# Performance work log

Hardware: AMD Instinct MI355X
Metric: run time of the kernel (lower is better)

The kernel has to match this reference:

```python
import jax, jax.numpy as jnp
import numpy as np

VOCAB = 50257
EMB = 512
HID = 1024
H = HID // 2  # per-direction hidden
TAGS = 24
START = 22
STOP = 23
SEQ = 4096
NEG = -10000.0


def setup_inputs() -> dict:
    key = jax.random.key(0)
    ks = jax.random.split(key, 16)
    s = 1.0 / np.sqrt(H)
    u = lambda k, shp: jax.random.uniform(k, shp, jnp.float32, -s, s)
    sentence = jax.random.randint(ks[0], (SEQ,), 0, VOCAB)
    emb = jax.random.normal(ks[1], (VOCAB, EMB), jnp.float32)
    w_ih_f = u(ks[2], (4 * H, EMB)); w_hh_f = u(ks[3], (4 * H, H))
    b_ih_f = u(ks[4], (4 * H,));    b_hh_f = u(ks[5], (4 * H,))
    w_ih_b = u(ks[6], (4 * H, EMB)); w_hh_b = u(ks[7], (4 * H, H))
    b_ih_b = u(ks[8], (4 * H,));    b_hh_b = u(ks[9], (4 * H,))
    w_tag = u(ks[10], (TAGS, HID)); b_tag = u(ks[11], (TAGS,))
    transitions = jax.random.normal(ks[12], (TAGS, TAGS), jnp.float32)
    transitions = transitions.at[START, :].set(NEG).at[:, STOP].set(NEG)
    h0 = jax.random.normal(ks[13], (2, H), jnp.float32)  # [dir, H]
    c0 = jax.random.normal(ks[14], (2, H), jnp.float32)
    return dict(sentence=sentence, emb=emb,
                w_ih_f=w_ih_f, w_hh_f=w_hh_f, b_ih_f=b_ih_f, b_hh_f=b_hh_f,
                w_ih_b=w_ih_b, w_hh_b=w_hh_b, b_ih_b=b_ih_b, b_hh_b=b_hh_b,
                w_tag=w_tag, b_tag=b_tag, transitions=transitions, h0=h0, c0=c0)


def _lstm_dir(x, w_ih, w_hh, b_ih, b_hh, h, c, reverse):
    # x: [T, EMB]; precompute input projections once
    xg = x @ w_ih.T + (b_ih + b_hh)  # [T, 4H]
    def step(carry, xt):
        h, c = carry
        g = xt + h @ w_hh.T
        i, f, gg, o = jnp.split(g, 4)
        i = jax.nn.sigmoid(i); f = jax.nn.sigmoid(f)
        gg = jnp.tanh(gg);     o = jax.nn.sigmoid(o)
        c = f * c + i * gg
        h = o * jnp.tanh(c)
        return (h, c), h
    _, hs = jax.lax.scan(step, (h, c), xg, reverse=reverse)
    return hs  # [T, H]


def reference(sentence, emb, w_ih_f, w_hh_f, b_ih_f, b_hh_f,
              w_ih_b, w_hh_b, b_ih_b, b_hh_b, w_tag, b_tag,
              transitions, h0, c0):
    x = emb[sentence]  # [T, EMB]
    hf = _lstm_dir(x, w_ih_f, w_hh_f, b_ih_f, b_hh_f, h0[0], c0[0], False)
    hb = _lstm_dir(x, w_ih_b, w_hh_b, b_ih_b, b_hh_b, h0[1], c0[1], True)
    lstm_out = jnp.concatenate([hf, hb], axis=-1)          # [T, HID]
    feats = lstm_out @ w_tag.T + b_tag                     # [T, TAGS]

    # Viterbi: max-plus recursion over tags, vectorized per timestep
    fv0 = jnp.full((TAGS,), NEG, jnp.float32).at[START].set(0.0)
    def vstep(fv, feat):
        scores = transitions + fv[None, :]                 # [next, prev]
        bp = jnp.argmax(scores, axis=1)
        return jnp.max(scores, axis=1) + feat, bp
    fv, bps = jax.lax.scan(vstep, fv0, feats)              # bps: [T, TAGS]

    terminal = fv + transitions[STOP]
    best = jnp.argmax(terminal)
    path_score = terminal[best]

    def btstep(tag, bp):
        prev = bp[tag]
        return prev, prev
    _, ys = jax.lax.scan(btstep, best, bps, reverse=True)  # ys[t] = tag at t-1; ys[0]==START
    best_path = jnp.concatenate([ys[1:], best[None]]).astype(jnp.int32)
    return path_score, best_path
```

## Files before the change

kernel.cpp:

```cpp
#include <hip/hip_runtime.h>
#include <cstdint>
#include <cstddef>

#define T_SEQ 4096
#define EMB_D 512
#define HDIM 512
#define G4 2048
#define NTAGS 24
#define START_TAG 22
#define STOP_TAG 23
#define NEGV -10000.0f
#define NBLK 32
#define HSLICE 16
#define SENT 0xFFFFFFFFu

__global__ __launch_bounds__(256) void gemm_xg_kernel(
    const int* __restrict__ sent, const float* __restrict__ emb,
    const float* __restrict__ w_ih_f, const float* __restrict__ b_ih_f, const float* __restrict__ b_hh_f,
    const float* __restrict__ w_ih_b, const float* __restrict__ b_ih_b, const float* __restrict__ b_hh_b,
    float* __restrict__ xg)
{
    const int dir = blockIdx.z;
    const float* W  = dir ? w_ih_b : w_ih_f;
    const float* bi = dir ? b_ih_b : b_ih_f;
    const float* bh = dir ? b_hh_b : b_hh_f;
    const int m0 = blockIdx.y * 64;
    const int n0 = blockIdx.x * 64;
    const int tid = threadIdx.x;

    __shared__ __attribute__((aligned(16))) float As[32][64];
    __shared__ __attribute__((aligned(16))) float Bs[32][64];

    const int lrow = tid >> 2;
    const int lk   = (tid & 3) * 8;

    const int srow = sent[m0 + lrow];
    const float* aptr = emb + (size_t)srow * EMB_D + lk;
    const float* bptr = W   + (size_t)(n0 + lrow) * EMB_D + lk;

    const int ty = tid >> 4;
    const int tx = tid & 15;

    float acc[4][4];
    #pragma unroll
    for (int i = 0; i < 4; ++i)
        #pragma unroll
        for (int j = 0; j < 4; ++j) acc[i][j] = 0.f;

    for (int kk = 0; kk < EMB_D; kk += 32) {
        float4 a0 = *(const float4*)(aptr + kk);
        float4 a1 = *(const float4*)(aptr + kk + 4);
        float4 b0 = *(const float4*)(bptr + kk);
        float4 b1 = *(const float4*)(bptr + kk + 4);
        __syncthreads();
        As[lk+0][lrow]=a0.x; As[lk+1][lrow]=a0.y; As[lk+2][lrow]=a0.z; As[lk+3][lrow]=a0.w;
        As[lk+4][lrow]=a1.x; As[lk+5][lrow]=a1.y; As[lk+6][lrow]=a1.z; As[lk+7][lrow]=a1.w;
        Bs[lk+0][lrow]=b0.x; Bs[lk+1][lrow]=b0.y; Bs[lk+2][lrow]=b0.z; Bs[lk+3][lrow]=b0.w;
        Bs[lk+4][lrow]=b1.x; Bs[lk+5][lrow]=b1.y; Bs[lk+6][lrow]=b1.z; Bs[lk+7][lrow]=b1.w;
        __syncthreads();
        #pragma unroll
        for (int k = 0; k < 32; ++k) {
            float4 av = *(const float4*)&As[k][ty*4];
            float4 bv = *(const float4*)&Bs[k][tx*4];
            acc[0][0]+=av.x*bv.x; acc[0][1]+=av.x*bv.y; acc[0][2]+=av.x*bv.z; acc[0][3]+=av.x*bv.w;
            acc[1][0]+=av.y*bv.x; acc[1][1]+=av.y*bv.y; acc[1][2]+=av.y*bv.z; acc[1][3]+=av.y*bv.w;
            acc[2][0]+=av.z*bv.x; acc[2][1]+=av.z*bv.y; acc[2][2]+=av.z*bv.z; acc[2][3]+=av.z*bv.w;
            acc[3][0]+=av.w*bv.x; acc[3][1]+=av.w*bv.y; acc[3][2]+=av.w*bv.z; acc[3][3]+=av.w*bv.w;
        }
    }
    #pragma unroll
    for (int i = 0; i < 4; ++i) {
        const int t = m0 + ty*4 + i;
        float* crow = xg + ((size_t)dir*T_SEQ + t) * G4 + n0 + tx*4;
        #pragma unroll
        for (int j = 0; j < 4; ++j) {
            const int jg = n0 + tx*4 + j;
            crow[j] = acc[i][j] + bi[jg] + bh[jg];
        }
    }
}

__global__ __attribute__((amdgpu_waves_per_eu(2, 2))) __launch_bounds__(512)
void bilstm_kernel(
    const float* __restrict__ w_hh_f, const float* __restrict__ w_hh_b,
    const float* __restrict__ h0, const float* __restrict__ c0,
    const float* __restrict__ xg,
    uint32_t* __restrict__ h_hist)
{
    const int blk = blockIdx.x;
    const int dir = blk >> 5;
    const int b   = blk & 31;
    const int tid = threadIdx.x;
    const int q   = tid >> 6;
    const int rl  = tid & 63;
    const int g2  = rl >> 4;
    const int hu  = rl & 15;
    const int row = g2 * HDIM + b * HSLICE + hu;

    const float* Wrow = (dir ? w_hh_b : w_hh_f) + (size_t)row * HDIM + q * 64;
    float4 w4[16];
    #pragma unroll
    for (int j = 0; j < 16; ++j) w4[j] = ((const float4*)Wrow)[j];

    __shared__ __attribute__((aligned(16))) float hbuf[512];
    __shared__ float part[512];

    float c = (tid < HSLICE) ? c0[dir*HDIM + b*HSLICE + tid] : 0.f;

    const float* xgd = xg + (size_t)dir * T_SEQ * G4;
    uint32_t* hh = h_hist + (size_t)dir * T_SEQ * HDIM;

    for (int idx = 0; idx < T_SEQ; ++idx) {
        const int t = dir ? (T_SEQ - 1 - idx) : idx;
        float xv = 0.f;
        if (tid < 64) xv = xgd[(size_t)t * G4 + row];

        if (idx == 0) {
            hbuf[tid] = h0[dir*HDIM + tid];
        } else {
            const int tprev = dir ? (t + 1) : (t - 1);
            const uint32_t* wp = hh + (size_t)tprev*HDIM + tid;
            uint32_t u;
            do {
                u = __hip_atomic_load(wp, __ATOMIC_RELAXED, __HIP_MEMORY_SCOPE_AGENT);
            } while (u == SENT);
            union { uint32_t u; float f; } cv; cv.u = u;
            hbuf[tid] = cv.f;
        }
        __syncthreads();

        float s = 0.f;
        const float4* hb4 = (const float4*)&hbuf[q*64];
        #pragma unroll
        for (int j = 0; j < 16; ++j) {
            float4 hv = hb4[j];
            s += w4[j].x*hv.x + w4[j].y*hv.y + w4[j].z*hv.z + w4[j].w*hv.w;
        }
        part[tid] = s;
        __syncthreads();

        if (tid < 64) {
            float g = xv;
            #pragma unroll
            for (int qq = 0; qq < 8; ++qq) g += part[qq*64 + tid];
            g = (g2 == 2) ? tanhf(g) : 1.f/(1.f + expf(-g));
            float iv = __shfl(g, hu);
            float fg = __shfl(g, hu + 16);
            float gv = __shfl(g, hu + 32);
            float ov = __shfl(g, hu + 48);
            if (tid < HSLICE) {
                c = fg*c + iv*gv;
                union { float f; uint32_t u; } hb; hb.f = ov * tanhf(c);
                __hip_atomic_store(hh + (size_t)t*HDIM + b*HSLICE + tid, hb.u,
                                   __ATOMIC_RELAXED, __HIP_MEMORY_SCOPE_AGENT);
            }
        }
    }
}

__global__ __launch_bounds__(256) void feats_kernel(
    const float* __restrict__ h_hist, const float* __restrict__ w_tag,
    const float* __restrict__ b_tag, float* __restrict__ feats)
{
    const int t = blockIdx.x;
    const int tid = threadIdx.x;
    __shared__ __attribute__((aligned(16))) float h[1024];
    __shared__ float partl[192];
    for (int i = tid; i < 512; i += 256) {
        h[i]     = h_hist[(size_t)t*HDIM + i];
        h[512+i] = h_hist[(size_t)T_SEQ*HDIM + (size_t)t*HDIM + i];
    }
    __syncthreads();
    if (tid < 192) {
        const int tag = tid >> 3, p = tid & 7;
        const float* wr = w_tag + (size_t)tag*1024 + p*128;
        const float* hp = h + p*128;
        float s = 0.f;
        #pragma unroll 8
        for (int j = 0; j < 128; ++j) s += wr[j]*hp[j];
        partl[tid] = s;
    }
    __syncthreads();
    if (tid < NTAGS) {
        float s = b_tag[tid];
        #pragma unroll
        for (int p = 0; p < 8; ++p) s += partl[tid*8+p];
        feats[(size_t)t*NTAGS + tid] = s;
    }
}

__global__ void viterbi_fwd_kernel(
    const float* __restrict__ feats, const float* __restrict__ trans,
    float* __restrict__ d_out, unsigned char* __restrict__ bp,
    int* __restrict__ best_tag)
{
    const int lane = threadIdx.x;
    const bool act = lane < NTAGS;
    float tr[NTAGS];
    #pragma unroll
    for (int p = 0; p < NTAGS; ++p)
        tr[p] = act ? trans[lane*NTAGS + p] : NEGV;

    float fv = (lane == START_TAG) ? 0.f : NEGV;
    __shared__ float fvs[NTAGS];
    __shared__ float term[NTAGS];

    float ftn = act ? feats[lane] : 0.f;
    for (int t = 0; t < T_SEQ; ++t) {
        if (act) fvs[lane] = fv;
        __syncthreads();
        float ft = ftn;
        if (act && t + 1 < T_SEQ) ftn = feats[(size_t)(t+1)*NTAGS + lane];
        float bestv = -3.4e38f;
        int argp = 0;
        #pragma unroll
        for (int p = 0; p < NTAGS; ++p) {
            float sc = tr[p] + fvs[p];
            if (sc > bestv) { bestv = sc; argp = p; }
        }
        __syncthreads();
        fv = bestv + ft;
        if (act) bp[(size_t)t*NTAGS + lane] = (unsigned char)argp;
    }
    if (act) { fv += trans[STOP_TAG*NTAGS + lane]; term[lane] = fv; }
    __syncthreads();
    if (lane == 0) {
        float bv = term[0]; int bi = 0;
        #pragma unroll
        for (int p = 1; p < NTAGS; ++p) if (term[p] > bv) { bv = term[p]; bi = p; }
        d_out[0] = bv;
        *best_tag = bi;
    }
}

__global__ void bt_compose_kernel(const unsigned char* __restrict__ bp,
                                  unsigned char* __restrict__ segmap)
{
    const int s = blockIdx.x;
    const int tid = threadIdx.x;
    __shared__ __attribute__((aligned(16))) unsigned char lbp[64*NTAGS];
    const uint32_t* src = (const uint32_t*)(bp + (size_t)s * 64 * NTAGS);
    uint32_t* dst = (uint32_t*)lbp;
    #pragma unroll
    for (int i = 0; i < 6; ++i) dst[tid + 64*i] = src[tid + 64*i];
    __syncthreads();
    if (tid < NTAGS) {
        int m = tid;
        for (int tt = 63; tt >= 0; --tt) m = lbp[tt*NTAGS + m];
        segmap[s*NTAGS + tid] = (unsigned char)m;
    }
}

__global__ void bt_final_kernel(const unsigned char* __restrict__ segmap,
                                const int* __restrict__ best_tag,
                                int* __restrict__ end_tags)
{
    if (threadIdx.x == 0) {
        int tag = *best_tag;
        end_tags[63] = tag;
        for (int s = 63; s >= 1; --s) {
            tag = segmap[s*NTAGS + tag];
            end_tags[s-1] = tag;
        }
    }
}

__global__ void bt_write_kernel(const unsigned char* __restrict__ bp,
                                const int* __restrict__ end_tags,
                                float* __restrict__ out_path)
{
    const int s = blockIdx.x;
    const int tid = threadIdx.x;
    __shared__ __attribute__((aligned(16))) unsigned char lbp[64*NTAGS];
    const uint32_t* src = (const uint32_t*)(bp + (size_t)s * 64 * NTAGS);
    uint32_t* dst = (uint32_t*)lbp;
    #pragma unroll
    for (int i = 0; i < 6; ++i) dst[tid + 64*i] = src[tid + 64*i];
    __syncthreads();
    if (tid == 0) {
        int tag = end_tags[s];
        out_path[s*64 + 63] = (float)tag;
        for (int tt = 63; tt >= 1; --tt) {
            tag = lbp[tt*NTAGS + tag];
            out_path[s*64 + tt - 1] = (float)tag;
        }
    }
}

extern "C" void kernel_launch(void* const* d_in, const int* in_sizes, int n_in,
                              void* d_out, int out_size, void* d_ws, size_t ws_size,
                              hipStream_t stream)
{
    const int*   sent   = (const int*)d_in[0];
    const float* emb    = (const float*)d_in[1];
    const float* w_ih_f = (const float*)d_in[2];
    const float* w_hh_f = (const float*)d_in[3];
    const float* b_ih_f = (const float*)d_in[4];
    const float* b_hh_f = (const float*)d_in[5];
    const float* w_ih_b = (const float*)d_in[6];
    const float* w_hh_b = (const float*)d_in[7];
    const float* b_ih_b = (const float*)d_in[8];
    const float* b_hh_b = (const float*)d_in[9];
    const float* w_tag  = (const float*)d_in[10];
    const float* b_tag  = (const float*)d_in[11];
    const float* trans  = (const float*)d_in[12];
    const float* h0     = (const float*)d_in[13];
    const float* c0     = (const float*)d_in[14];
    float* out = (float*)d_out;

    char* ws = (char*)d_ws;
    size_t off = 0;
    auto alloc = [&](size_t bytes) {
        char* p = ws + off; off += (bytes + 255) & ~(size_t)255; return p;
    };
    float* xg      = (float*)alloc((size_t)2*T_SEQ*G4*sizeof(float));
    uint32_t* h_hist = (uint32_t*)alloc((size_t)2*T_SEQ*HDIM*sizeof(float));
    float* feats   = (float*)alloc((size_t)T_SEQ*NTAGS*sizeof(float));
    unsigned char* bp     = (unsigned char*)alloc((size_t)T_SEQ*NTAGS);
    unsigned char* segmap = (unsigned char*)alloc(64*NTAGS);
    int* best_tag = (int*)alloc(sizeof(int));
    int* end_tags = (int*)alloc(64*sizeof(int));

    if (off > ws_size) {
        hipMemsetAsync(d_out, 0xFF, 4, stream);
        return;
    }

    hipMemsetAsync(h_hist, 0xFF, (size_t)2*T_SEQ*HDIM*sizeof(float), stream);

    dim3 gg(G4/64, T_SEQ/64, 2);
    gemm_xg_kernel<<<gg, 256, 0, stream>>>(sent, emb,
        w_ih_f, b_ih_f, b_hh_f, w_ih_b, b_ih_b, b_hh_b, xg);
    bilstm_kernel<<<64, 512, 0, stream>>>(w_hh_f, w_hh_b, h0, c0, xg, h_hist);
    feats_kernel<<<T_SEQ, 256, 0, stream>>>((const float*)h_hist, w_tag, b_tag, feats);
    viterbi_fwd_kernel<<<1, 64, 0, stream>>>(feats, trans, out, bp, best_tag);
    bt_compose_kernel<<<64, 64, 0, stream>>>(bp, segmap);
    bt_final_kernel<<<1, 64, 0, stream>>>(segmap, best_tag, end_tags);
    bt_write_kernel<<<64, 64, 0, stream>>>(bp, end_tags, out + 1);
}
```

Before: 9.430 ms.

## Pin each LSTM direction's blocks to a single XCC via dynamic rank claiming

Launches 512 blocks, reads the hardware XCC ID, and lets only the first 32 blocks landing on XCC 0 (forward) and XCC 1 (backward) run the recurrence; all others exit. This keeps every block of a direction's step-to-step h exchange on one XCC, so the spin-wait polling and stores meet in a shared L2 instead of crossing dies. It also forces the recurrent weights to stay in VGPRs through an empty asm barrier. The risk is that it depends on the hardware block-to-XCC placement: if fewer than 32 co-resident blocks land on an XCC, the spin-waits could deadlock. The extra launched blocks also add overhead.

```diff
diff --git a/kernel.cpp b/kernel.cpp
--- a/kernel.cpp
+++ b/kernel.cpp
@@ -85,11 +85,27 @@
     const float* __restrict__ w_hh_f, const float* __restrict__ w_hh_b,
     const float* __restrict__ h0, const float* __restrict__ c0,
     const float* __restrict__ xg,
-    uint32_t* __restrict__ h_hist)
-{
-    const int blk = blockIdx.x;
-    const int dir = blk >> 5;
-    const int b   = blk & 31;
+    uint32_t* __restrict__ h_hist,
+    int* __restrict__ claim)
+{
+    uint32_t xcc;
+    asm volatile("s_getreg_b32 %0, hwreg(HW_REG_XCC_ID)" : "=s"(xcc));
+    xcc &= 7u;
+
+    __shared__ int rank_s;
+    if (threadIdx.x == 0)
+        rank_s = __hip_atomic_fetch_add(&claim[xcc], 1, __ATOMIC_RELAXED,
+                                        __HIP_MEMORY_SCOPE_AGENT);
+    __syncthreads();
+    const int rank = rank_s;
+
+    int dir;
+    if (xcc == 0) dir = 0;
+    else if (xcc == 1) dir = 1;
+    else return;
+    if (rank >= NBLK) return;
+    const int b = rank;
+
     const int tid = threadIdx.x;
     const int q   = tid >> 6;
     const int rl  = tid & 63;
@@ -98,9 +114,14 @@
     const int row = g2 * HDIM + b * HSLICE + hu;
 
     const float* Wrow = (dir ? w_hh_b : w_hh_f) + (size_t)row * HDIM + q * 64;
-    float4 w4[16];
-    #pragma unroll
-    for (int j = 0; j < 16; ++j) w4[j] = ((const float4*)Wrow)[j];
+    float w[64];
+    #pragma unroll
+    for (int j = 0; j < 16; ++j) {
+        float4 v = ((const float4*)Wrow)[j];
+        w[4*j+0]=v.x; w[4*j+1]=v.y; w[4*j+2]=v.z; w[4*j+3]=v.w;
+    }
+    #pragma unroll
+    for (int i = 0; i < 64; ++i) asm volatile("" : "+v"(w[i]));
 
     __shared__ __attribute__((aligned(16))) float hbuf[512];
     __shared__ float part[512];
@@ -134,7 +155,7 @@
         #pragma unroll
         for (int j = 0; j < 16; ++j) {
             float4 hv = hb4[j];
-            s += w4[j].x*hv.x + w4[j].y*hv.y + w4[j].z*hv.z + w4[j].w*hv.w;
+            s += w[4*j+0]*hv.x + w[4*j+1]*hv.y + w[4*j+2]*hv.z + w[4*j+3]*hv.w;
         }
         part[tid] = s;
         __syncthreads();
@@ -320,6 +341,7 @@
     unsigned char* segmap = (unsigned char*)alloc(64*NTAGS);
     int* best_tag = (int*)alloc(sizeof(int));
     int* end_tags = (int*)alloc(64*sizeof(int));
+    int* claim    = (int*)alloc(8*sizeof(int));
 
     if (off > ws_size) {
         hipMemsetAsync(d_out, 0xFF, 4, stream);
@@ -327,11 +349,12 @@
     }
 
     hipMemsetAsync(h_hist, 0xFF, (size_t)2*T_SEQ*HDIM*sizeof(float), stream);
+    hipMemsetAsync(claim, 0, 8*sizeof(int), stream);
 
     dim3 gg(G4/64, T_SEQ/64, 2);
     gemm_xg_kernel<<<gg, 256, 0, stream>>>(sent, emb,
         w_ih_f, b_ih_f, b_hh_f, w_ih_b, b_ih_b, b_hh_b, xg);
-    bilstm_kernel<<<64, 512, 0, stream>>>(w_hh_f, w_hh_b, h0, c0, xg, h_hist);
+    bilstm_kernel<<<512, 512, 0, stream>>>(w_hh_f, w_hh_b, h0, c0, xg, h_hist, claim);
     feats_kernel<<<T_SEQ, 256, 0, stream>>>((const float*)h_hist, w_tag, b_tag, feats);
     viterbi_fwd_kernel<<<1, 64, 0, stream>>>(feats, trans, out, bp, best_tag);
     bt_compose_kernel<<<64, 64, 0, stream>>>(bp, segmap);
```

Measured after the change: 8.697 ms. -7.8%, faster.
